# Kernel optimization log

Measured on AMD Instinct MI355X. Metric: run time of the kernel, lower is better.

The kernel has to match this reference:

```python
import jax, jax.numpy as jnp
import numpy as np

EMB = 64
HID = 128
N_NODES = 50000
N_EDGES = 800000
N_Q = 64

def setup_inputs() -> dict:
    key = jax.random.key(0)
    ks = jax.random.split(key, 20)
    d = {}
    d['question_emb'] = jax.random.normal(ks[0], (N_Q, EMB), dtype=jnp.float32)
    d['node_embeddings'] = jax.random.normal(ks[1], (N_NODES, EMB), dtype=jnp.float32)
    d['edge_embeddings'] = jax.random.normal(ks[2], (N_EDGES, EMB), dtype=jnp.float32)
    d['edge_index'] = jax.random.randint(ks[3], (2, N_EDGES), 0, N_NODES, dtype=jnp.int32)
    d['node_batch'] = jnp.sort(jax.random.randint(ks[4], (N_NODES,), 0, N_Q, dtype=jnp.int32))
    s = 1.0 / np.sqrt(EMB)
    # projector weights (Linear emb->emb), stored as (in, out)
    d['Wq'] = jax.random.normal(ks[5], (EMB, EMB), dtype=jnp.float32) * s
    d['bq'] = jnp.zeros((EMB,), dtype=jnp.float32)
    d['We'] = jax.random.normal(ks[6], (EMB, EMB), dtype=jnp.float32) * s
    d['be'] = jnp.zeros((EMB,), dtype=jnp.float32)
    d['Wr'] = jax.random.normal(ks[7], (EMB, EMB), dtype=jnp.float32) * s
    d['br'] = jnp.zeros((EMB,), dtype=jnp.float32)
    # DenseFeatureExtractor: concat(4*EMB) -> EMB -> HID, ReLU after each
    d['W1'] = jax.random.normal(ks[8], (4 * EMB, EMB), dtype=jnp.float32) / np.sqrt(4 * EMB)
    d['b1'] = jnp.zeros((EMB,), dtype=jnp.float32)
    d['W2'] = jax.random.normal(ks[9], (EMB, HID), dtype=jnp.float32) * s
    d['b2'] = jnp.zeros((HID,), dtype=jnp.float32)
    # DeterministicHead: HID -> 1
    d['Wh'] = jax.random.normal(ks[10], (HID, 1), dtype=jnp.float32) / np.sqrt(HID)
    d['bh'] = jnp.zeros((1,), dtype=jnp.float32)
    return d


def reference(question_emb, node_embeddings, edge_embeddings, edge_index, node_batch,
              Wq, bq, We, be, Wr, br, W1, b1, W2, b2, Wh, bh):
    head_idx, tail_idx = edge_index[0], edge_index[1]
    query_ids = node_batch[head_idx]                       # [E]
    # projections (applied to the small tables, then gathered per edge)
    q_repr = question_emb @ Wq + bq                        # [Q, D]
    node_repr = node_embeddings @ We + be                  # [N, D]
    rel_repr = edge_embeddings @ Wr + br                   # [E, D]
    semantic = jnp.concatenate([
        q_repr[query_ids], node_repr[head_idx], rel_repr, node_repr[tail_idx]
    ], axis=-1)                                            # [E, 4D]
    h = jax.nn.relu(semantic @ W1 + b1)                    # [E, D]
    h = jax.nn.relu(h @ W2 + b2)                           # [E, H]
    logits = (h @ Wh + bh)[:, 0]                           # [E]
    scores = jax.nn.sigmoid(logits)
    return scores
```

## Files before the change

kernel.cpp:

```cpp
#include <hip/hip_runtime.h>

#define NNODE 50000
#define NEDGE 800000

typedef __attribute__((ext_vector_type(8))) short bf16x8;
typedef __attribute__((ext_vector_type(4))) float f32x4;

#define WB_QCB   0
#define WB_WRTB  8192
#define WB_W2TB  16384
#define WB_WEH   33024
#define WB_WET   49408
#define WB_NHB   65792
#define WB_NTB   6465792

__device__ inline ushort f2b(float x) {
    uint u = __float_as_uint(x);
    return (ushort)((u + 0x7fffu + ((u >> 16) & 1u)) >> 16);
}
__device__ inline float bLo(uint u) { return __uint_as_float(u << 16); }
__device__ inline float bHi(uint u) { return __uint_as_float(u & 0xffff0000u); }

__device__ inline void bar_lds() {
    asm volatile("s_waitcnt lgkmcnt(0)" ::: "memory");
    __builtin_amdgcn_s_barrier();
    asm volatile("" ::: "memory");
}

__device__ inline void stage64(float* dst, const float* __restrict__ src, int t) {
    #pragma unroll
    for (int i = 0; i < 4; ++i) {
        int f = t + i * 256;
        *(float4*)&dst[f * 4] = *(const float4*)&src[f * 4];
    }
}

__device__ inline void gemm64(const float* sA, const float* sB, int t, float acc[4][4]) {
    const int r0 = (t >> 4) * 4, c0 = (t & 15) * 4;
    #pragma unroll
    for (int j = 0; j < 4; ++j)
        #pragma unroll
        for (int i = 0; i < 4; ++i) acc[j][i] = 0.f;
    #pragma unroll 4
    for (int k = 0; k < 64; ++k) {
        float4 b = *(const float4*)&sB[k * 64 + c0];
        float bv[4] = {b.x, b.y, b.z, b.w};
        #pragma unroll
        for (int j = 0; j < 4; ++j) {
            float a = sA[(r0 + j) * 64 + k];
            #pragma unroll
            for (int i = 0; i < 4; ++i) acc[j][i] = fmaf(a, bv[i], acc[j][i]);
        }
    }
}

__global__ __launch_bounds__(256)
void prep_small(const float* __restrict__ Q,
                const float* __restrict__ Wq, const float* __restrict__ bq,
                const float* __restrict__ We, const float* __restrict__ be,
                const float* __restrict__ Wr, const float* __restrict__ br,
                const float* __restrict__ W1, const float* __restrict__ b1,
                const float* __restrict__ W2, char* __restrict__ wsb)
{
    __shared__ float sA[4096], sB[4096], sC[4096], sBias[64];
    const int t = threadIdx.x;
    const int bid = blockIdx.x;
    const int r0 = (t >> 4) * 4, c0 = (t & 15) * 4;

    if (bid == 0) {
        stage64(sA, Wq, t); stage64(sB, W1, t);
        __syncthreads();
        float acc[4][4];
        gemm64(sA, sB, t, acc);
        #pragma unroll
        for (int j = 0; j < 4; ++j)
            *(float4*)&sC[(r0 + j) * 64 + c0] = make_float4(acc[j][0], acc[j][1], acc[j][2], acc[j][3]);
        if (t < 64) {
            float s = b1[t];
            for (int k = 0; k < 64; ++k) {
                s = fmaf(bq[k], W1[k * 64 + t], s);
                s = fmaf(be[k], W1[(64 + k) * 64 + t] + W1[(192 + k) * 64 + t], s);
                s = fmaf(br[k], W1[(128 + k) * 64 + t], s);
            }
            sBias[t] = s;
        }
        __syncthreads();
        stage64(sA, Q, t);
        __syncthreads();
        gemm64(sA, sC, t, acc);
        ushort* qcb = (ushort*)(wsb + WB_QCB);
        #pragma unroll
        for (int j = 0; j < 4; ++j) {
            ushort4 p;
            p.x = f2b(acc[j][0] + sBias[c0 + 0]);
            p.y = f2b(acc[j][1] + sBias[c0 + 1]);
            p.z = f2b(acc[j][2] + sBias[c0 + 2]);
            p.w = f2b(acc[j][3] + sBias[c0 + 3]);
            *(ushort4*)&qcb[(r0 + j) * 64 + c0] = p;
        }
    } else if (bid == 1 || bid == 2) {
        const float* w1seg = W1 + (bid == 1 ? 64 * 64 : 192 * 64);
        float* dst = (float*)(wsb + (bid == 1 ? WB_WEH : WB_WET));
        stage64(sA, We, t); stage64(sB, w1seg, t);
        __syncthreads();
        float acc[4][4];
        gemm64(sA, sB, t, acc);
        #pragma unroll
        for (int j = 0; j < 4; ++j)
            *(float4*)&dst[(r0 + j) * 64 + c0] = make_float4(acc[j][0], acc[j][1], acc[j][2], acc[j][3]);
    } else if (bid == 3) {
        stage64(sA, Wr, t); stage64(sB, W1 + 128 * 64, t);
        __syncthreads();
        float acc[4][4];
        gemm64(sA, sB, t, acc);
        ushort* wrtb = (ushort*)(wsb + WB_WRTB);
        #pragma unroll
        for (int j = 0; j < 4; ++j)
            #pragma unroll
            for (int i = 0; i < 4; ++i)
                wrtb[(c0 + i) * 64 + (r0 + j)] = f2b(acc[j][i]);
    } else {
        ushort* w2tb = (ushort*)(wsb + WB_W2TB);
        #pragma unroll
        for (int i = 0; i < 32; ++i) {
            int f = t + i * 256;
            int k = f >> 7, n = f & 127;
            w2tb[n * 64 + k] = f2b(W2[f]);
        }
    }
}

__global__ __launch_bounds__(256)
void prep_nodes(const float* __restrict__ Xn, const char* __restrict__ wsb_c,
                char* __restrict__ wsb)
{
    __shared__ float sXT[64 * 68];
    __shared__ float sWeh[4096], sWet[4096];
    const int t = threadIdx.x;
    const int nbase = blockIdx.x * 64;
    const float* Weh = (const float*)(wsb_c + WB_WEH);
    const float* Wet = (const float*)(wsb_c + WB_WET);
    ushort* nhb = (ushort*)(wsb + WB_NHB);
    ushort* ntb = (ushort*)(wsb + WB_NTB);

    #pragma unroll
    for (int i = 0; i < 4; ++i) {
        int f = t + i * 256;
        int n = f >> 4, s4 = (f & 15) * 4;
        int gn = nbase + n;
        float4 v = make_float4(0.f, 0.f, 0.f, 0.f);
        if (gn < NNODE) v = *(const float4*)&Xn[gn * 64 + s4];
        sXT[(s4 + 0) * 68 + n] = v.x;
        sXT[(s4 + 1) * 68 + n] = v.y;
        sXT[(s4 + 2) * 68 + n] = v.z;
        sXT[(s4 + 3) * 68 + n] = v.w;
    }
    #pragma unroll
    for (int i = 0; i < 4; ++i) {
        int f = t + i * 256;
        *(float4*)&sWeh[f * 4] = *(const float4*)&Weh[f * 4];
        *(float4*)&sWet[f * 4] = *(const float4*)&Wet[f * 4];
    }
    __syncthreads();

    const int er = (t >> 4) * 4, cc = (t & 15) * 4;
    float ah[4][4], at[4][4];
    #pragma unroll
    for (int j = 0; j < 4; ++j)
        #pragma unroll
        for (int i = 0; i < 4; ++i) { ah[j][i] = 0.f; at[j][i] = 0.f; }
    #pragma unroll 4
    for (int k = 0; k < 64; ++k) {
        float4 a  = *(const float4*)&sXT[k * 68 + er];
        float4 bh = *(const float4*)&sWeh[k * 64 + cc];
        float4 bt = *(const float4*)&sWet[k * 64 + cc];
        float av[4] = {a.x, a.y, a.z, a.w};
        #pragma unroll
        for (int j = 0; j < 4; ++j) {
            ah[j][0] = fmaf(av[j], bh.x, ah[j][0]); ah[j][1] = fmaf(av[j], bh.y, ah[j][1]);
            ah[j][2] = fmaf(av[j], bh.z, ah[j][2]); ah[j][3] = fmaf(av[j], bh.w, ah[j][3]);
            at[j][0] = fmaf(av[j], bt.x, at[j][0]); at[j][1] = fmaf(av[j], bt.y, at[j][1]);
            at[j][2] = fmaf(av[j], bt.z, at[j][2]); at[j][3] = fmaf(av[j], bt.w, at[j][3]);
        }
    }
    #pragma unroll
    for (int j = 0; j < 4; ++j) {
        int n = nbase + er + j;
        if (n < NNODE) {
            ushort4 ph, pt;
            ph.x = f2b(ah[j][0]); ph.y = f2b(ah[j][1]); ph.z = f2b(ah[j][2]); ph.w = f2b(ah[j][3]);
            pt.x = f2b(at[j][0]); pt.y = f2b(at[j][1]); pt.z = f2b(at[j][2]); pt.w = f2b(at[j][3]);
            *(ushort4*)&nhb[n * 64 + cc] = ph;
            *(ushort4*)&ntb[n * 64 + cc] = pt;
        }
    }
}

#define TILES_PER_BLK 4

__global__ __launch_bounds__(256, 3)
void edge_kernel(const float* __restrict__ Xe,
                 const int* __restrict__ EI,
                 const int* __restrict__ NB,
                 const float* __restrict__ b2,
                 const float* __restrict__ Wh,
                 const float* __restrict__ bh,
                 const char* __restrict__ wsb,
                 float* __restrict__ out)
{
    __shared__ ushort sX[64 * 72];
    __shared__ ushort sWr[64 * 72];
    __shared__ ushort sW2[128 * 72];
    __shared__ ushort sG[64 * 72];
    __shared__ float  sB2s[128], sWhs[128];

    const int t = threadIdx.x;
    const ushort* qcb  = (const ushort*)(wsb + WB_QCB);
    const ushort* wrtb = (const ushort*)(wsb + WB_WRTB);
    const ushort* w2tb = (const ushort*)(wsb + WB_W2TB);
    const ushort* nhb  = (const ushort*)(wsb + WB_NHB);
    const ushort* ntb  = (const ushort*)(wsb + WB_NTB);

    const int eg  = t >> 2;
    const int c0g = (t & 3) * 16;

    {
        uint4 wrl[2], w2l[4];
        #pragma unroll
        for (int i = 0; i < 2; ++i) {
            int f = t + i * 256;
            wrl[i] = *(const uint4*)&wrtb[(f >> 3) * 64 + (f & 7) * 8];
        }
        #pragma unroll
        for (int i = 0; i < 4; ++i) {
            int f = t + i * 256;
            w2l[i] = *(const uint4*)&w2tb[(f >> 3) * 64 + (f & 7) * 8];
        }
        #pragma unroll
        for (int i = 0; i < 2; ++i) {
            int f = t + i * 256;
            *(uint4*)&sWr[(f >> 3) * 72 + (f & 7) * 8] = wrl[i];
        }
        #pragma unroll
        for (int i = 0; i < 4; ++i) {
            int f = t + i * 256;
            *(uint4*)&sW2[(f >> 3) * 72 + (f & 7) * 8] = w2l[i];
        }
        if (t < 128) { sB2s[t] = b2[t]; sWhs[t] = Wh[t]; }
    }
    const float bh0 = bh[0];

    auto load_tile = [&](int eb, uint4* g, float4* x) {
        int hd = EI[eb + eg];
        int tl = EI[NEDGE + eb + eg];
        int qi = NB[hd];
        g[0] = *(const uint4*)&qcb[qi * 64 + c0g];
        g[1] = *(const uint4*)&qcb[qi * 64 + c0g + 8];
        g[2] = *(const uint4*)&nhb[hd * 64 + c0g];
        g[3] = *(const uint4*)&nhb[hd * 64 + c0g + 8];
        g[4] = *(const uint4*)&ntb[tl * 64 + c0g];
        g[5] = *(const uint4*)&ntb[tl * 64 + c0g + 8];
        #pragma unroll
        for (int i = 0; i < 4; ++i) {
            int f = t + i * 256;
            x[i] = *(const float4*)&Xe[(eb + (f >> 4)) * 64 + (f & 15) * 4];
        }
    };

    int ebase = blockIdx.x * (64 * TILES_PER_BLK);
    uint4  g[6];  float4 x[4];
    uint4  ng[6]; float4 nx[4];
    load_tile(ebase, g, x);

    const int lane = t & 63;
    const int w = t >> 6;
    const int m = lane & 15;
    const int qq = lane >> 4;
    const int q8 = qq * 8;

    #pragma unroll
    for (int tile = 0; tile < TILES_PER_BLK; ++tile) {
        {
            uint pk[8];
            const uint* ua = (const uint*)&g[0];
            const uint* ub = (const uint*)&g[2];
            const uint* uc = (const uint*)&g[4];
            #pragma unroll
            for (int j = 0; j < 4; ++j) {
                float lo = bLo(ua[j]) + bLo(ub[j]) + bLo(uc[j]);
                float hi = bHi(ua[j]) + bHi(ub[j]) + bHi(uc[j]);
                pk[j] = (uint)f2b(lo) | ((uint)f2b(hi) << 16);
            }
            ua = (const uint*)&g[1]; ub = (const uint*)&g[3]; uc = (const uint*)&g[5];
            #pragma unroll
            for (int j = 0; j < 4; ++j) {
                float lo = bLo(ua[j]) + bLo(ub[j]) + bLo(uc[j]);
                float hi = bHi(ua[j]) + bHi(ub[j]) + bHi(uc[j]);
                pk[4 + j] = (uint)f2b(lo) | ((uint)f2b(hi) << 16);
            }
            *(uint4*)&sG[eg * 72 + c0g]     = make_uint4(pk[0], pk[1], pk[2], pk[3]);
            *(uint4*)&sG[eg * 72 + c0g + 8] = make_uint4(pk[4], pk[5], pk[6], pk[7]);
        }
        #pragma unroll
        for (int i = 0; i < 4; ++i) {
            int f = t + i * 256;
            int e = f >> 4, s4 = (f & 15) * 4;
            uint lo = (uint)f2b(x[i].x) | ((uint)f2b(x[i].y) << 16);
            uint hi = (uint)f2b(x[i].z) | ((uint)f2b(x[i].w) << 16);
            *(uint2*)&sX[e * 72 + s4] = make_uint2(lo, hi);
        }
        if (tile < TILES_PER_BLK - 1) load_tile(ebase + 64, ng, nx);
        bar_lds();

        bf16x8 a0 = *(const bf16x8*)&sX[(w * 16 + m) * 72 + q8];
        bf16x8 a1 = *(const bf16x8*)&sX[(w * 16 + m) * 72 + 32 + q8];
        f32x4 acc1[4];
        #pragma unroll
        for (int nt = 0; nt < 4; ++nt) {
            bf16x8 b0  = *(const bf16x8*)&sWr[(nt * 16 + m) * 72 + q8];
            bf16x8 b1v = *(const bf16x8*)&sWr[(nt * 16 + m) * 72 + 32 + q8];
            f32x4 c = {0.f, 0.f, 0.f, 0.f};
            c = __builtin_amdgcn_mfma_f32_16x16x32_bf16(a0, b0, c, 0, 0, 0);
            c = __builtin_amdgcn_mfma_f32_16x16x32_bf16(a1, b1v, c, 0, 0, 0);
            acc1[nt] = c;
        }
        ushort h1s[4][4];
        #pragma unroll
        for (int nt = 0; nt < 4; ++nt) {
            int c = nt * 16 + m;
            #pragma unroll
            for (int r = 0; r < 4; ++r) {
                int e = w * 16 + qq * 4 + r;
                float gv = __uint_as_float(((uint)sG[e * 72 + c]) << 16);
                h1s[nt][r] = f2b(fmaxf(acc1[nt][r] + gv, 0.f));
            }
        }
        bar_lds();
        #pragma unroll
        for (int nt = 0; nt < 4; ++nt) {
            int c = nt * 16 + m;
            #pragma unroll
            for (int r = 0; r < 4; ++r) {
                int e = w * 16 + qq * 4 + r;
                sX[e * 72 + c] = h1s[nt][r];
            }
        }
        bar_lds();

        bf16x8 A0 = *(const bf16x8*)&sX[(w * 16 + m) * 72 + q8];
        bf16x8 A1 = *(const bf16x8*)&sX[(w * 16 + m) * 72 + 32 + q8];
        float part[4] = {0.f, 0.f, 0.f, 0.f};
        #pragma unroll
        for (int nt = 0; nt < 8; ++nt) {
            bf16x8 B0 = *(const bf16x8*)&sW2[(nt * 16 + m) * 72 + q8];
            bf16x8 B1 = *(const bf16x8*)&sW2[(nt * 16 + m) * 72 + 32 + q8];
            f32x4 c = {0.f, 0.f, 0.f, 0.f};
            c = __builtin_amdgcn_mfma_f32_16x16x32_bf16(A0, B0, c, 0, 0, 0);
            c = __builtin_amdgcn_mfma_f32_16x16x32_bf16(A1, B1, c, 0, 0, 0);
            int col = nt * 16 + m;
            float b2v = sB2s[col], whv = sWhs[col];
            #pragma unroll
            for (int r = 0; r < 4; ++r)
                part[r] = fmaf(fmaxf(c[r] + b2v, 0.f), whv, part[r]);
        }
        #pragma unroll
        for (int md = 1; md < 16; md <<= 1) {
            part[0] += __shfl_xor(part[0], md, 64);
            part[1] += __shfl_xor(part[1], md, 64);
            part[2] += __shfl_xor(part[2], md, 64);
            part[3] += __shfl_xor(part[3], md, 64);
        }
        if (m == 0) {
            float4 o;
            o.x = 1.f / (1.f + __expf(-(part[0] + bh0)));
            o.y = 1.f / (1.f + __expf(-(part[1] + bh0)));
            o.z = 1.f / (1.f + __expf(-(part[2] + bh0)));
            o.w = 1.f / (1.f + __expf(-(part[3] + bh0)));
            *(float4*)&out[ebase + w * 16 + qq * 4] = o;
        }

        if (tile < TILES_PER_BLK - 1) {
            bar_lds();
            ebase += 64;
            #pragma unroll
            for (int i = 0; i < 6; ++i) g[i] = ng[i];
            #pragma unroll
            for (int i = 0; i < 4; ++i) x[i] = nx[i];
        }
    }
}

extern "C" void kernel_launch(void* const* d_in, const int* in_sizes, int n_in,
                              void* d_out, int out_size, void* d_ws, size_t ws_size,
                              hipStream_t stream)
{
    const float* Q   = (const float*)d_in[0];
    const float* Xn  = (const float*)d_in[1];
    const float* Xe  = (const float*)d_in[2];
    const int*   EI  = (const int*)d_in[3];
    const int*   NB  = (const int*)d_in[4];
    const float* Wq  = (const float*)d_in[5];
    const float* bq  = (const float*)d_in[6];
    const float* We  = (const float*)d_in[7];
    const float* be  = (const float*)d_in[8];
    const float* Wr  = (const float*)d_in[9];
    const float* br  = (const float*)d_in[10];
    const float* W1  = (const float*)d_in[11];
    const float* b1  = (const float*)d_in[12];
    const float* W2  = (const float*)d_in[13];
    const float* b2  = (const float*)d_in[14];
    const float* Wh  = (const float*)d_in[15];
    const float* bh  = (const float*)d_in[16];
    float* out = (float*)d_out;
    char*  wsb = (char*)d_ws;

    prep_small<<<5, 256, 0, stream>>>(Q, Wq, bq, We, be, Wr, br, W1, b1, W2, wsb);
    prep_nodes<<<(NNODE + 63) / 64, 256, 0, stream>>>(Xn, wsb, wsb);
    edge_kernel<<<NEDGE / (64 * TILES_PER_BLK), 256, 0, stream>>>(Xe, EI, NB, b2, Wh, bh, wsb, out);
}
```

Before: 360.7 us.

## Make per-tile LDS staging wave-local and drop block barriers

Remaps the edge-embedding staging so each wave loads and writes only the 16 sX rows it later reads, matching the already wave-local sG rows. With no cross-wave sharing of per-tile LDS data, all per-tile block barriers are removed and the h1 activations are written straight back into sX. Bias and head weights move from shared memory into per-thread registers. This relies on in-order LDS access within a wave and on the compiler keeping the store/load order, and it slightly raises register use.

```diff
diff --git a/kernel.cpp b/kernel.cpp
--- a/kernel.cpp
+++ b/kernel.cpp
@@ -20,12 +20,6 @@
 }
 __device__ inline float bLo(uint u) { return __uint_as_float(u << 16); }
 __device__ inline float bHi(uint u) { return __uint_as_float(u & 0xffff0000u); }
-
-__device__ inline void bar_lds() {
-    asm volatile("s_waitcnt lgkmcnt(0)" ::: "memory");
-    __builtin_amdgcn_s_barrier();
-    asm volatile("" ::: "memory");
-}
 
 __device__ inline void stage64(float* dst, const float* __restrict__ src, int t) {
     #pragma unroll
@@ -212,7 +206,6 @@
     __shared__ ushort sWr[64 * 72];
     __shared__ ushort sW2[128 * 72];
     __shared__ ushort sG[64 * 72];
-    __shared__ float  sB2s[128], sWhs[128];
 
     const int t = threadIdx.x;
     const ushort* qcb  = (const ushort*)(wsb + WB_QCB);
@@ -221,8 +214,16 @@
     const ushort* nhb  = (const ushort*)(wsb + WB_NHB);
     const ushort* ntb  = (const ushort*)(wsb + WB_NTB);
 
+    const int lane = t & 63;
+    const int w    = t >> 6;
+    const int m    = lane & 15;
+    const int qq   = lane >> 4;
+    const int q8   = qq * 8;
+
     const int eg  = t >> 2;
     const int c0g = (t & 3) * 16;
+    const int xrow = 16 * w + (lane >> 2);
+    const int xsl  = lane & 3;
 
     {
         uint4 wrl[2], w2l[4];
@@ -246,9 +247,16 @@
             int f = t + i * 256;
             *(uint4*)&sW2[(f >> 3) * 72 + (f & 7) * 8] = w2l[i];
         }
-        if (t < 128) { sB2s[t] = b2[t]; sWhs[t] = Wh[t]; }
+    }
+    float b2v[8], whv[8];
+    #pragma unroll
+    for (int nt = 0; nt < 8; ++nt) {
+        b2v[nt] = b2[nt * 16 + m];
+        whv[nt] = Wh[nt * 16 + m];
     }
     const float bh0 = bh[0];
+
+    __syncthreads();
 
     auto load_tile = [&](int eb, uint4* g, float4* x) {
         int hd = EI[eb + eg];
@@ -261,22 +269,14 @@
         g[4] = *(const uint4*)&ntb[tl * 64 + c0g];
         g[5] = *(const uint4*)&ntb[tl * 64 + c0g + 8];
         #pragma unroll
-        for (int i = 0; i < 4; ++i) {
-            int f = t + i * 256;
-            x[i] = *(const float4*)&Xe[(eb + (f >> 4)) * 64 + (f & 15) * 4];
-        }
+        for (int i = 0; i < 4; ++i)
+            x[i] = *(const float4*)&Xe[(eb + xrow) * 64 + (xsl + 4 * i) * 4];
     };
 
     int ebase = blockIdx.x * (64 * TILES_PER_BLK);
     uint4  g[6];  float4 x[4];
     uint4  ng[6]; float4 nx[4];
     load_tile(ebase, g, x);
-
-    const int lane = t & 63;
-    const int w = t >> 6;
-    const int m = lane & 15;
-    const int qq = lane >> 4;
-    const int q8 = qq * 8;
 
     #pragma unroll
     for (int tile = 0; tile < TILES_PER_BLK; ++tile) {
@@ -303,14 +303,11 @@
         }
         #pragma unroll
         for (int i = 0; i < 4; ++i) {
-            int f = t + i * 256;
-            int e = f >> 4, s4 = (f & 15) * 4;
             uint lo = (uint)f2b(x[i].x) | ((uint)f2b(x[i].y) << 16);
             uint hi = (uint)f2b(x[i].z) | ((uint)f2b(x[i].w) << 16);
-            *(uint2*)&sX[e * 72 + s4] = make_uint2(lo, hi);
+            *(uint2*)&sX[xrow * 72 + (xsl + 4 * i) * 4] = make_uint2(lo, hi);
         }
         if (tile < TILES_PER_BLK - 1) load_tile(ebase + 64, ng, nx);
-        bar_lds();
 
         bf16x8 a0 = *(const bf16x8*)&sX[(w * 16 + m) * 72 + q8];
         bf16x8 a1 = *(const bf16x8*)&sX[(w * 16 + m) * 72 + 32 + q8];
@@ -324,7 +321,6 @@
             c = __builtin_amdgcn_mfma_f32_16x16x32_bf16(a1, b1v, c, 0, 0, 0);
             acc1[nt] = c;
         }
-        ushort h1s[4][4];
         #pragma unroll
         for (int nt = 0; nt < 4; ++nt) {
             int c = nt * 16 + m;
@@ -332,20 +328,9 @@
             for (int r = 0; r < 4; ++r) {
                 int e = w * 16 + qq * 4 + r;
                 float gv = __uint_as_float(((uint)sG[e * 72 + c]) << 16);
-                h1s[nt][r] = f2b(fmaxf(acc1[nt][r] + gv, 0.f));
+                sX[e * 72 + c] = f2b(fmaxf(acc1[nt][r] + gv, 0.f));
             }
         }
-        bar_lds();
-        #pragma unroll
-        for (int nt = 0; nt < 4; ++nt) {
-            int c = nt * 16 + m;
-            #pragma unroll
-            for (int r = 0; r < 4; ++r) {
-                int e = w * 16 + qq * 4 + r;
-                sX[e * 72 + c] = h1s[nt][r];
-            }
-        }
-        bar_lds();
 
         bf16x8 A0 = *(const bf16x8*)&sX[(w * 16 + m) * 72 + q8];
         bf16x8 A1 = *(const bf16x8*)&sX[(w * 16 + m) * 72 + 32 + q8];
@@ -357,11 +342,9 @@
             f32x4 c = {0.f, 0.f, 0.f, 0.f};
             c = __builtin_amdgcn_mfma_f32_16x16x32_bf16(A0, B0, c, 0, 0, 0);
             c = __builtin_amdgcn_mfma_f32_16x16x32_bf16(A1, B1, c, 0, 0, 0);
-            int col = nt * 16 + m;
-            float b2v = sB2s[col], whv = sWhs[col];
             #pragma unroll
             for (int r = 0; r < 4; ++r)
-                part[r] = fmaf(fmaxf(c[r] + b2v, 0.f), whv, part[r]);
+                part[r] = fmaf(fmaxf(c[r] + b2v[nt], 0.f), whv[nt], part[r]);
         }
         #pragma unroll
         for (int md = 1; md < 16; md <<= 1) {
@@ -380,7 +363,6 @@
         }
 
         if (tile < TILES_PER_BLK - 1) {
-            bar_lds();
             ebase += 64;
             #pragma unroll
             for (int i = 0; i < 6; ++i) g[i] = ng[i];
```

Measured after the change: 360.2 us. No clear change (-0.1%).
